# Optimization experiments

Hardware: AMD Instinct MI355X
Metric: run time of the kernel (lower is better)

## Reference

```python
import jax, jax.numpy as jnp
import numpy as np

N, DIM, K = 50000, 64, 16
POS_HID = 64
ATTN_HID = DIM * 4


def setup_inputs() -> dict:
    key = jax.random.key(0)
    ks = jax.random.split(key, 12)
    s = lambda fan_in: 1.0 / np.sqrt(fan_in)
    return {
        "x": jax.random.normal(ks[0], (N, DIM), jnp.float32),
        "pos": jax.random.normal(ks[1], (N, 3), jnp.float32),
        "attn_index": jax.random.randint(ks[2], (N, K), 0, N),
        "mask": jnp.zeros((N, K), dtype=bool),
        "w_qkv": jax.random.normal(ks[3], (DIM, 3 * DIM), jnp.float32) * s(DIM),
        "pm_w1": jax.random.normal(ks[4], (3, POS_HID), jnp.float32) * s(3),
        "pm_b1": jnp.zeros((POS_HID,), jnp.float32),
        "pm_w2": jax.random.normal(ks[5], (POS_HID, DIM), jnp.float32) * s(POS_HID),
        "pm_b2": jnp.zeros((DIM,), jnp.float32),
        "am_w1": jax.random.normal(ks[6], (DIM, ATTN_HID), jnp.float32) * s(DIM),
        "am_b1": jnp.zeros((ATTN_HID,), jnp.float32),
        "am_w2": jax.random.normal(ks[7], (ATTN_HID, DIM), jnp.float32) * s(ATTN_HID),
        "am_b2": jnp.zeros((DIM,), jnp.float32),
    }


def reference(x, pos, attn_index, mask, w_qkv, pm_w1, pm_b1, pm_w2, pm_b2,
              am_w1, am_b1, am_w2, am_b2):
    # qkv projection and split: [N, dim] each
    qkv = x @ w_qkv
    x_q, x_k, x_v = jnp.split(qkv, 3, axis=-1)

    # gather neighbors: [N, K, dim] / [N, K, 3]
    x_k = x_k[attn_index]
    x_v = x_v[attn_index]
    rel_pos = pos[attn_index] - pos[:, None, :]

    # positional MLP: 3 -> POS_HID -> dim
    rel = jax.nn.relu(rel_pos @ pm_w1 + pm_b1) @ pm_w2 + pm_b2

    # attention MLP on (k - q + rel): dim -> 4*dim -> dim
    w = x_k - x_q[:, None, :] + rel
    w = jax.nn.relu(w @ am_w1 + am_b1) @ am_w2 + am_b2

    # masked softmax over the neighbor dim (axis=1), per channel
    w = jnp.where(mask[:, :, None], -jnp.inf, w)
    w = jax.nn.softmax(w, axis=1)

    # weighted aggregation: [N, dim]
    agg = jnp.sum((x_v + rel) * w, axis=1)
    return agg
```

## Files before the change

### kernel.cpp

```cpp
#include <hip/hip_runtime.h>
#include <hip/hip_bf16.h>
#include <math.h>
#include <stdint.h>

#define DIM   64
#define KNB   16
#define QKVW  192
#define RVP   72
#define TFP   24

typedef short bf16x8 __attribute__((ext_vector_type(8)));
typedef float f32x4  __attribute__((ext_vector_type(4)));

__device__ __forceinline__ short f2bf_s(float x) {
    return (short)__builtin_bit_cast(unsigned short, __float2bfloat16(x));
}
__device__ __forceinline__ float bf2f(uint16_t u) {
    uint32_t v = ((uint32_t)u) << 16;
    return __builtin_bit_cast(float, v);
}

__global__ __launch_bounds__(256) void prep_kernel(
    const float* __restrict__ x, const float* __restrict__ wqkv,
    const float* __restrict__ am_w1, const float* __restrict__ am_w2,
    const float* __restrict__ pm_w2,
    uint16_t* __restrict__ qkvp, uint16_t* __restrict__ w1p,
    uint16_t* __restrict__ w2p, uint16_t* __restrict__ pw2p,
    int n, int nqkvb)
{
    const int tid = threadIdx.x;
    if (blockIdx.x < nqkvb) {
        const int w4   = tid >> 6;
        const int lane = tid & 63;
        const int g    = lane >> 4;
        const int nb   = lane & 15;
        const int r0   = blockIdx.x * 16;
        const int rowA = min(r0 + nb, n - 1);

        bf16x8 af[2];
#pragma unroll
        for (int kt = 0; kt < 2; ++kt) {
            const float* xr = x + (size_t)rowA * 64 + 32 * kt + 8 * g;
            const float4 a0 = *(const float4*)xr;
            const float4 a1 = *(const float4*)(xr + 4);
            bf16x8 f;
            f[0] = f2bf_s(a0.x); f[1] = f2bf_s(a0.y); f[2] = f2bf_s(a0.z); f[3] = f2bf_s(a0.w);
            f[4] = f2bf_s(a1.x); f[5] = f2bf_s(a1.y); f[6] = f2bf_s(a1.z); f[7] = f2bf_s(a1.w);
            af[kt] = f;
        }

#pragma unroll
        for (int t = 0; t < 3; ++t) {
            const int nt  = 3 * w4 + t;
            const int col = 16 * nt + nb;
            bf16x8 b0, b1;
#pragma unroll
            for (int j = 0; j < 8; ++j) {
                b0[j] = f2bf_s(wqkv[(8 * g + j) * QKVW + col]);
                b1[j] = f2bf_s(wqkv[(32 + 8 * g + j) * QKVW + col]);
            }
            f32x4 acc = {0.f, 0.f, 0.f, 0.f};
            acc = __builtin_amdgcn_mfma_f32_16x16x32_bf16(af[0], b0, acc, 0, 0, 0);
            acc = __builtin_amdgcn_mfma_f32_16x16x32_bf16(af[1], b1, acc, 0, 0, 0);
#pragma unroll
            for (int r = 0; r < 4; ++r) {
                const int row = r0 + 4 * g + r;
                if (row < n)
                    qkvp[(size_t)row * QKVW + col] = (uint16_t)f2bf_s(acc[r]);
            }
        }
    } else {
        int t = (blockIdx.x - nqkvb) * 256 + tid;
        if (t >= 36864) return;
        int j = t & 7, lane = (t >> 3) & 63, tile = t >> 9;
        int g = lane >> 4, nb = lane & 15;
        if (tile < 32) {
            int mt = tile >> 1, kt = tile & 1;
            w1p[t] = (uint16_t)f2bf_s(am_w1[(32 * kt + 8 * g + j) * 256 + 16 * mt + nb]);
        } else if (tile < 64) {
            int tt = tile - 32;
            int mt = tt >> 3, kt = tt & 7;
            w2p[t - 16384] = (uint16_t)f2bf_s(am_w2[(32 * kt + 8 * g + j) * 64 + 16 * mt + nb]);
        } else {
            int tt = tile - 64;
            int nt = tt >> 1, kt = tt & 1;
            pw2p[t - 32768] = (uint16_t)f2bf_s(pm_w2[(32 * kt + 8 * g + j) * 64 + 16 * nt + nb]);
        }
    }
}

__global__ __launch_bounds__(256, 2) void ptl_main(
    const float* __restrict__ pos,
    const int* __restrict__ aidx,
    const uint8_t* __restrict__ mask,
    const float* __restrict__ pm_w1,
    const float* __restrict__ pm_b1,
    const float* __restrict__ pm_b2,
    const float* __restrict__ am_b1,
    const uint16_t* __restrict__ qkvp,
    const uint16_t* __restrict__ w1p,
    const uint16_t* __restrict__ w2p,
    const uint16_t* __restrict__ pw2p,
    float* __restrict__ out,
    int npts)
{
    const int tid  = threadIdx.x;
    const int w    = tid >> 6;
    const int lane = tid & 63;
    const int g    = lane >> 4;
    const int nb   = lane & 15;

    __shared__ alignas(16) uint16_t s_rel[4][16][RVP];
    __shared__ alignas(16) uint16_t s_vrel[64][RVP];
    __shared__ alignas(16) uint16_t s_h2[64][256];
    __shared__ alignas(16) uint16_t s_tf[4][64][TFP];

    bf16x8 aw1[4][2], aw2[8];
#pragma unroll
    for (int m = 0; m < 4; ++m)
#pragma unroll
        for (int kt = 0; kt < 2; ++kt)
            aw1[m][kt] = *(const bf16x8*)(w1p + (size_t)(((4 * w + m) * 2 + kt) * 64 + lane) * 8);
#pragma unroll
    for (int kt = 0; kt < 8; ++kt)
        aw2[kt] = *(const bf16x8*)(w2p + (size_t)((w * 8 + kt) * 64 + lane) * 8);

    const int ngroups = (npts + 3) >> 2;

    int   pnw;
    float cx, cy, cz, prx, pry, prz;
    bf16x8 pk0, pk1;
    uint16_t pqv[4];

    auto stage_load = [&](int gbn) {
        const int gcl = min(gbn, ngroups - 1);
        const int ipn = min(gcl * 4 + w, npts - 1);
        pnw = aidx[ipn * KNB + nb];
        cx = pos[3 * ipn]; cy = pos[3 * ipn + 1]; cz = pos[3 * ipn + 2];
        prx = pos[3 * pnw]; pry = pos[3 * pnw + 1]; prz = pos[3 * pnw + 2];
        pk0 = *(const bf16x8*)(qkvp + (size_t)pnw * QKVW + 64 + 8 * g);
        pk1 = *(const bf16x8*)(qkvp + (size_t)pnw * QKVW + 96 + 8 * g);
#pragma unroll
        for (int nt = 0; nt < 4; ++nt)
            pqv[nt] = qkvp[(size_t)ipn * QKVW + 16 * nt + nb];
    };

    stage_load(blockIdx.x);

    for (int gb = blockIdx.x; gb < ngroups; gb += gridDim.x) {
        const int i0  = gb * 4;
        const int ipw = min(i0 + w, npts - 1);

        {
            const float rx = prx - cx, ry = pry - cy, rz = prz - cz;

            bf16x8 h1f[2];
#pragma unroll
            for (int kt = 0; kt < 2; ++kt) {
                const int hb = 32 * kt + 8 * g;
                float w0[8], w1r[8], w2r[8], bb[8];
                *(float4*)&w0[0]  = *(const float4*)(pm_w1 + hb);
                *(float4*)&w0[4]  = *(const float4*)(pm_w1 + hb + 4);
                *(float4*)&w1r[0] = *(const float4*)(pm_w1 + 64 + hb);
                *(float4*)&w1r[4] = *(const float4*)(pm_w1 + 64 + hb + 4);
                *(float4*)&w2r[0] = *(const float4*)(pm_w1 + 128 + hb);
                *(float4*)&w2r[4] = *(const float4*)(pm_w1 + 128 + hb + 4);
                *(float4*)&bb[0]  = *(const float4*)(pm_b1 + hb);
                *(float4*)&bb[4]  = *(const float4*)(pm_b1 + hb + 4);
                bf16x8 f;
#pragma unroll
                for (int jj = 0; jj < 8; ++jj) {
                    float v = fmaf(rx, w0[jj], fmaf(ry, w1r[jj], fmaf(rz, w2r[jj], bb[jj])));
                    f[jj] = f2bf_s(fmaxf(v, 0.f));
                }
                h1f[kt] = f;
            }
#pragma unroll
            for (int nt = 0; nt < 4; ++nt) {
                const bf16x8 b0 = *(const bf16x8*)(pw2p + (size_t)((nt * 2 + 0) * 64 + lane) * 8);
                const bf16x8 b1 = *(const bf16x8*)(pw2p + (size_t)((nt * 2 + 1) * 64 + lane) * 8);
                f32x4 acc = {0.f, 0.f, 0.f, 0.f};
                acc = __builtin_amdgcn_mfma_f32_16x16x32_bf16(h1f[0], b0, acc, 0, 0, 0);
                acc = __builtin_amdgcn_mfma_f32_16x16x32_bf16(h1f[1], b1, acc, 0, 0, 0);
                const int ch = 16 * nt + nb;
                const float bias = pm_b2[ch];
                const float qv = bf2f(pqv[nt]);
#pragma unroll
                for (int r = 0; r < 4; ++r)
                    s_rel[w][4 * g + r][ch] = (uint16_t)f2bf_s(acc[r] + bias - qv);
            }

            const bf16x8 rl0 = *(const bf16x8*)&s_rel[w][nb][8 * g];
            const bf16x8 rl1 = *(const bf16x8*)&s_rel[w][nb][32 + 8 * g];
            bf16x8 tf0, tf1;
#pragma unroll
            for (int j = 0; j < 8; ++j) {
                tf0[j] = f2bf_s(bf2f((uint16_t)pk0[j]) + bf2f((uint16_t)rl0[j]));
                tf1[j] = f2bf_s(bf2f((uint16_t)pk1[j]) + bf2f((uint16_t)rl1[j]));
            }
            *(bf16x8*)&s_tf[w][lane][0] = tf0;
            *(bf16x8*)&s_tf[w][lane][8] = tf1;
        }
        __syncthreads();

        {
            const bf16x8 pv0 = *(const bf16x8*)(qkvp + (size_t)pnw * QKVW + 128 + 8 * g);
            const bf16x8 pv1 = *(const bf16x8*)(qkvp + (size_t)pnw * QKVW + 160 + 8 * g);
            const bf16x8 pq0 = *(const bf16x8*)(qkvp + (size_t)ipw * QKVW + 8 * g);
            const bf16x8 pq1 = *(const bf16x8*)(qkvp + (size_t)ipw * QKVW + 32 + 8 * g);

#pragma unroll
            for (int pt = 0; pt < 4; ++pt) {
                const bf16x8 tf0 = *(const bf16x8*)&s_tf[pt][lane][0];
                const bf16x8 tf1 = *(const bf16x8*)&s_tf[pt][lane][8];

                f32x4 hacc[4];
                __builtin_amdgcn_s_setprio(1);
#pragma unroll
                for (int m = 0; m < 4; ++m) {
                    f32x4 a = {0.f, 0.f, 0.f, 0.f};
                    a = __builtin_amdgcn_mfma_f32_16x16x32_bf16(aw1[m][0], tf0, a, 0, 0, 0);
                    a = __builtin_amdgcn_mfma_f32_16x16x32_bf16(aw1[m][1], tf1, a, 0, 0, 0);
                    hacc[m] = a;
                }
                __builtin_amdgcn_s_setprio(0);
#pragma unroll
                for (int m = 0; m < 4; ++m) {
                    const int hb = 16 * (4 * w + m) + 4 * g;
                    const float4 b4 = *(const float4*)(am_b1 + hb);
                    const uint32_t lo = (uint32_t)(uint16_t)f2bf_s(fmaxf(hacc[m][0] + b4.x, 0.f))
                                      | ((uint32_t)(uint16_t)f2bf_s(fmaxf(hacc[m][1] + b4.y, 0.f)) << 16);
                    const uint32_t hi = (uint32_t)(uint16_t)f2bf_s(fmaxf(hacc[m][2] + b4.z, 0.f))
                                      | ((uint32_t)(uint16_t)f2bf_s(fmaxf(hacc[m][3] + b4.w, 0.f)) << 16);
                    const int sl = (2 * (4 * w + m) + (g >> 1)) ^ (nb & 7);
                    *(uint2*)((char*)&s_h2[16 * pt + nb][0] + sl * 16 + 8 * (g & 1)) = make_uint2(lo, hi);
                }
            }

            {
                const bf16x8 rl0 = *(const bf16x8*)&s_rel[w][nb][8 * g];
                const bf16x8 rl1 = *(const bf16x8*)&s_rel[w][nb][32 + 8 * g];
                bf16x8 va, vb;
#pragma unroll
                for (int j = 0; j < 8; ++j) {
                    va[j] = f2bf_s(bf2f((uint16_t)pv0[j]) + bf2f((uint16_t)rl0[j]) + bf2f((uint16_t)pq0[j]));
                    vb[j] = f2bf_s(bf2f((uint16_t)pv1[j]) + bf2f((uint16_t)rl1[j]) + bf2f((uint16_t)pq1[j]));
                }
                *(bf16x8*)&s_vrel[16 * w + nb][8 * g]      = va;
                *(bf16x8*)&s_vrel[16 * w + nb][32 + 8 * g] = vb;
            }
        }
        __syncthreads();

        stage_load(gb + gridDim.x);

#pragma unroll
        for (int mt = 0; mt < 4; ++mt) {
            const int ip  = i0 + mt;
            const int ipc = min(ip, npts - 1);

            f32x4 wacc = {0.f, 0.f, 0.f, 0.f};
            __builtin_amdgcn_s_setprio(1);
#pragma unroll
            for (int kt = 0; kt < 8; ++kt) {
                const int sl = (4 * kt + g) ^ (nb & 7);
                const bf16x8 a = *(const bf16x8*)((const char*)&s_h2[16 * mt + nb][0] + sl * 16);
                wacc = __builtin_amdgcn_mfma_f32_16x16x32_bf16(a, aw2[kt], wacc, 0, 0, 0);
            }
            __builtin_amdgcn_s_setprio(0);

            const uchar4 m4 = *(const uchar4*)(mask + (size_t)ipc * KNB + 4 * g);
            const float sc0 = m4.x ? -INFINITY : wacc[0];
            const float sc1 = m4.y ? -INFINITY : wacc[1];
            const float sc2 = m4.z ? -INFINITY : wacc[2];
            const float sc3 = m4.w ? -INFINITY : wacc[3];
            float mx = fmaxf(fmaxf(sc0, sc1), fmaxf(sc2, sc3));
            mx = fmaxf(mx, __shfl_xor(mx, 16));
            mx = fmaxf(mx, __shfl_xor(mx, 32));
            const float e0 = __expf(sc0 - mx), e1 = __expf(sc1 - mx);
            const float e2 = __expf(sc2 - mx), e3 = __expf(sc3 - mx);
            float den = (e0 + e1) + (e2 + e3);

            const int vc = 16 * w + nb;
            const float vr0 = bf2f(s_vrel[16 * mt + 4 * g + 0][vc]);
            const float vr1 = bf2f(s_vrel[16 * mt + 4 * g + 1][vc]);
            const float vr2 = bf2f(s_vrel[16 * mt + 4 * g + 2][vc]);
            const float vr3 = bf2f(s_vrel[16 * mt + 4 * g + 3][vc]);
            float num = e0 * vr0;
            num = fmaf(e1, vr1, num);
            num = fmaf(e2, vr2, num);
            num = fmaf(e3, vr3, num);

            den += __shfl_xor(den, 16); den += __shfl_xor(den, 32);
            num += __shfl_xor(num, 16); num += __shfl_xor(num, 32);
            if (lane < 16 && ip < npts)
                out[(size_t)ip * 64 + vc] = __fdividef(num, den);
        }
    }
}

extern "C" void kernel_launch(void* const* d_in, const int* in_sizes, int n_in,
                              void* d_out, int out_size, void* d_ws, size_t ws_size,
                              hipStream_t stream) {
    const float*   x     = (const float*)d_in[0];
    const float*   pos   = (const float*)d_in[1];
    const int*     aidx  = (const int*)d_in[2];
    const uint8_t* mask  = (const uint8_t*)d_in[3];
    const float*   wqkv  = (const float*)d_in[4];
    const float*   pm_w1 = (const float*)d_in[5];
    const float*   pm_b1 = (const float*)d_in[6];
    const float*   pm_w2 = (const float*)d_in[7];
    const float*   pm_b2 = (const float*)d_in[8];
    const float*   am_w1 = (const float*)d_in[9];
    const float*   am_b1 = (const float*)d_in[10];
    const float*   am_w2 = (const float*)d_in[11];
    float* out = (float*)d_out;
    const int n = in_sizes[0] / DIM;

    uint8_t* ws = (uint8_t*)d_ws;
    uint16_t* qkvp = (uint16_t*)ws;
    uint16_t* w1p  = (uint16_t*)(ws + (size_t)n * QKVW * 2);
    uint16_t* w2p  = w1p + 16384;
    uint16_t* pw2p = w2p + 16384;

    const int nqkvb = (n + 15) / 16;
    prep_kernel<<<nqkvb + 144, 256, 0, stream>>>(x, wqkv, am_w1, am_w2, pm_w2,
                                                 qkvp, w1p, w2p, pw2p, n, nqkvb);
    ptl_main<<<512, 256, 0, stream>>>(pos, aidx, mask, pm_w1, pm_b1, pm_b2, am_b1,
                                      qkvp, w1p, w2p, pw2p, out, n);
}
```

Before: 160.0 us.

## Halve hidden-activation LDS buffer and process points in two phases for occupancy

The per-block hidden-activation shared buffer is halved and the s_tf row padding is reduced, cutting LDS per block so more blocks fit per CU. The grid grows from 512 to 768 blocks to use the extra occupancy. To make the smaller buffer work, the first-MLP/MFMA stage and the second-MLP/softmax stage now each run on two points at a time, alternating, with the v+rel staging split by wave halves. The cost is two extra block barriers per iteration, and the tighter s_tf padding may add LDS bank conflicts.

```diff
diff --git a/kernel.cpp b/kernel.cpp
--- a/kernel.cpp
+++ b/kernel.cpp
@@ -7,7 +7,7 @@
 #define KNB   16
 #define QKVW  192
 #define RVP   72
-#define TFP   24
+#define TFP   16
 
 typedef short bf16x8 __attribute__((ext_vector_type(8)));
 typedef float f32x4  __attribute__((ext_vector_type(4)));
@@ -112,7 +112,7 @@
 
     __shared__ alignas(16) uint16_t s_rel[4][16][RVP];
     __shared__ alignas(16) uint16_t s_vrel[64][RVP];
-    __shared__ alignas(16) uint16_t s_h2[64][256];
+    __shared__ alignas(16) uint16_t s_h2h[32][256];
     __shared__ alignas(16) uint16_t s_tf[4][64][TFP];
 
     bf16x8 aw1[4][2], aw2[8];
@@ -150,6 +150,103 @@
     for (int gb = blockIdx.x; gb < ngroups; gb += gridDim.x) {
         const int i0  = gb * 4;
         const int ipw = min(i0 + w, npts - 1);
+
+        auto P2half = [&](int pt0) {
+            const bool own = (w & 2) == pt0;
+            bf16x8 pv0_, pv1_, pq0_, pq1_;
+            if (own) {
+                pv0_ = *(const bf16x8*)(qkvp + (size_t)pnw * QKVW + 128 + 8 * g);
+                pv1_ = *(const bf16x8*)(qkvp + (size_t)pnw * QKVW + 160 + 8 * g);
+                pq0_ = *(const bf16x8*)(qkvp + (size_t)ipw * QKVW + 8 * g);
+                pq1_ = *(const bf16x8*)(qkvp + (size_t)ipw * QKVW + 32 + 8 * g);
+            }
+#pragma unroll
+            for (int ptl = 0; ptl < 2; ++ptl) {
+                const int pt = pt0 + ptl;
+                const bf16x8 tf0 = *(const bf16x8*)&s_tf[pt][lane][0];
+                const bf16x8 tf1 = *(const bf16x8*)&s_tf[pt][lane][8];
+
+                f32x4 hacc[4];
+                __builtin_amdgcn_s_setprio(1);
+#pragma unroll
+                for (int m = 0; m < 4; ++m) {
+                    f32x4 a = {0.f, 0.f, 0.f, 0.f};
+                    a = __builtin_amdgcn_mfma_f32_16x16x32_bf16(aw1[m][0], tf0, a, 0, 0, 0);
+                    a = __builtin_amdgcn_mfma_f32_16x16x32_bf16(aw1[m][1], tf1, a, 0, 0, 0);
+                    hacc[m] = a;
+                }
+                __builtin_amdgcn_s_setprio(0);
+#pragma unroll
+                for (int m = 0; m < 4; ++m) {
+                    const int hb = 16 * (4 * w + m) + 4 * g;
+                    const float4 b4 = *(const float4*)(am_b1 + hb);
+                    const uint32_t lo = (uint32_t)(uint16_t)f2bf_s(fmaxf(hacc[m][0] + b4.x, 0.f))
+                                      | ((uint32_t)(uint16_t)f2bf_s(fmaxf(hacc[m][1] + b4.y, 0.f)) << 16);
+                    const uint32_t hi = (uint32_t)(uint16_t)f2bf_s(fmaxf(hacc[m][2] + b4.z, 0.f))
+                                      | ((uint32_t)(uint16_t)f2bf_s(fmaxf(hacc[m][3] + b4.w, 0.f)) << 16);
+                    const int sl = (2 * (4 * w + m) + (g >> 1)) ^ (nb & 7);
+                    *(uint2*)((char*)&s_h2h[16 * ptl + nb][0] + sl * 16 + 8 * (g & 1)) = make_uint2(lo, hi);
+                }
+            }
+            if (own) {
+                const bf16x8 rl0 = *(const bf16x8*)&s_rel[w][nb][8 * g];
+                const bf16x8 rl1 = *(const bf16x8*)&s_rel[w][nb][32 + 8 * g];
+                bf16x8 va, vb;
+#pragma unroll
+                for (int j = 0; j < 8; ++j) {
+                    va[j] = f2bf_s(bf2f((uint16_t)pv0_[j]) + bf2f((uint16_t)rl0[j]) + bf2f((uint16_t)pq0_[j]));
+                    vb[j] = f2bf_s(bf2f((uint16_t)pv1_[j]) + bf2f((uint16_t)rl1[j]) + bf2f((uint16_t)pq1_[j]));
+                }
+                *(bf16x8*)&s_vrel[16 * w + nb][8 * g]      = va;
+                *(bf16x8*)&s_vrel[16 * w + nb][32 + 8 * g] = vb;
+            }
+        };
+
+        auto P3half = [&](int pt0) {
+#pragma unroll
+            for (int mi = 0; mi < 2; ++mi) {
+                const int mt  = pt0 + mi;
+                const int ip  = i0 + mt;
+                const int ipc = min(ip, npts - 1);
+
+                f32x4 wacc = {0.f, 0.f, 0.f, 0.f};
+                __builtin_amdgcn_s_setprio(1);
+#pragma unroll
+                for (int kt = 0; kt < 8; ++kt) {
+                    const int sl = (4 * kt + g) ^ (nb & 7);
+                    const bf16x8 a = *(const bf16x8*)((const char*)&s_h2h[16 * mi + nb][0] + sl * 16);
+                    wacc = __builtin_amdgcn_mfma_f32_16x16x32_bf16(a, aw2[kt], wacc, 0, 0, 0);
+                }
+                __builtin_amdgcn_s_setprio(0);
+
+                const uchar4 m4 = *(const uchar4*)(mask + (size_t)ipc * KNB + 4 * g);
+                const float sc0 = m4.x ? -INFINITY : wacc[0];
+                const float sc1 = m4.y ? -INFINITY : wacc[1];
+                const float sc2 = m4.z ? -INFINITY : wacc[2];
+                const float sc3 = m4.w ? -INFINITY : wacc[3];
+                float mx = fmaxf(fmaxf(sc0, sc1), fmaxf(sc2, sc3));
+                mx = fmaxf(mx, __shfl_xor(mx, 16));
+                mx = fmaxf(mx, __shfl_xor(mx, 32));
+                const float e0 = __expf(sc0 - mx), e1 = __expf(sc1 - mx);
+                const float e2 = __expf(sc2 - mx), e3 = __expf(sc3 - mx);
+                float den = (e0 + e1) + (e2 + e3);
+
+                const int vc = 16 * w + nb;
+                const float vr0 = bf2f(s_vrel[16 * mt + 4 * g + 0][vc]);
+                const float vr1 = bf2f(s_vrel[16 * mt + 4 * g + 1][vc]);
+                const float vr2 = bf2f(s_vrel[16 * mt + 4 * g + 2][vc]);
+                const float vr3 = bf2f(s_vrel[16 * mt + 4 * g + 3][vc]);
+                float num = e0 * vr0;
+                num = fmaf(e1, vr1, num);
+                num = fmaf(e2, vr2, num);
+                num = fmaf(e3, vr3, num);
+
+                den += __shfl_xor(den, 16); den += __shfl_xor(den, 32);
+                num += __shfl_xor(num, 16); num += __shfl_xor(num, 32);
+                if (lane < 16 && ip < npts)
+                    out[(size_t)ip * 64 + vc] = __fdividef(num, den);
+            }
+        };
 
         {
             const float rx = prx - cx, ry = pry - cy, rz = prz - cz;
@@ -203,99 +300,14 @@
         }
         __syncthreads();
 
-        {
-            const bf16x8 pv0 = *(const bf16x8*)(qkvp + (size_t)pnw * QKVW + 128 + 8 * g);
-            const bf16x8 pv1 = *(const bf16x8*)(qkvp + (size_t)pnw * QKVW + 160 + 8 * g);
-            const bf16x8 pq0 = *(const bf16x8*)(qkvp + (size_t)ipw * QKVW + 8 * g);
-            const bf16x8 pq1 = *(const bf16x8*)(qkvp + (size_t)ipw * QKVW + 32 + 8 * g);
-
-#pragma unroll
-            for (int pt = 0; pt < 4; ++pt) {
-                const bf16x8 tf0 = *(const bf16x8*)&s_tf[pt][lane][0];
-                const bf16x8 tf1 = *(const bf16x8*)&s_tf[pt][lane][8];
-
-                f32x4 hacc[4];
-                __builtin_amdgcn_s_setprio(1);
-#pragma unroll
-                for (int m = 0; m < 4; ++m) {
-                    f32x4 a = {0.f, 0.f, 0.f, 0.f};
-                    a = __builtin_amdgcn_mfma_f32_16x16x32_bf16(aw1[m][0], tf0, a, 0, 0, 0);
-                    a = __builtin_amdgcn_mfma_f32_16x16x32_bf16(aw1[m][1], tf1, a, 0, 0, 0);
-                    hacc[m] = a;
-                }
-                __builtin_amdgcn_s_setprio(0);
-#pragma unroll
-                for (int m = 0; m < 4; ++m) {
-                    const int hb = 16 * (4 * w + m) + 4 * g;
-                    const float4 b4 = *(const float4*)(am_b1 + hb);
-                    const uint32_t lo = (uint32_t)(uint16_t)f2bf_s(fmaxf(hacc[m][0] + b4.x, 0.f))
-                                      | ((uint32_t)(uint16_t)f2bf_s(fmaxf(hacc[m][1] + b4.y, 0.f)) << 16);
-                    const uint32_t hi = (uint32_t)(uint16_t)f2bf_s(fmaxf(hacc[m][2] + b4.z, 0.f))
-                                      | ((uint32_t)(uint16_t)f2bf_s(fmaxf(hacc[m][3] + b4.w, 0.f)) << 16);
-                    const int sl = (2 * (4 * w + m) + (g >> 1)) ^ (nb & 7);
-                    *(uint2*)((char*)&s_h2[16 * pt + nb][0] + sl * 16 + 8 * (g & 1)) = make_uint2(lo, hi);
-                }
-            }
-
-            {
-                const bf16x8 rl0 = *(const bf16x8*)&s_rel[w][nb][8 * g];
-                const bf16x8 rl1 = *(const bf16x8*)&s_rel[w][nb][32 + 8 * g];
-                bf16x8 va, vb;
-#pragma unroll
-                for (int j = 0; j < 8; ++j) {
-                    va[j] = f2bf_s(bf2f((uint16_t)pv0[j]) + bf2f((uint16_t)rl0[j]) + bf2f((uint16_t)pq0[j]));
-                    vb[j] = f2bf_s(bf2f((uint16_t)pv1[j]) + bf2f((uint16_t)rl1[j]) + bf2f((uint16_t)pq1[j]));
-                }
-                *(bf16x8*)&s_vrel[16 * w + nb][8 * g]      = va;
-                *(bf16x8*)&s_vrel[16 * w + nb][32 + 8 * g] = vb;
-            }
-        }
+        P2half(0);
         __syncthreads();
-
+        P3half(0);
+        __syncthreads();
+        P2half(2);
+        __syncthreads();
         stage_load(gb + gridDim.x);
-
-#pragma unroll
-        for (int mt = 0; mt < 4; ++mt) {
-            const int ip  = i0 + mt;
-            const int ipc = min(ip, npts - 1);
-
-            f32x4 wacc = {0.f, 0.f, 0.f, 0.f};
-            __builtin_amdgcn_s_setprio(1);
-#pragma unroll
-            for (int kt = 0; kt < 8; ++kt) {
-                const int sl = (4 * kt + g) ^ (nb & 7);
-                const bf16x8 a = *(const bf16x8*)((const char*)&s_h2[16 * mt + nb][0] + sl * 16);
-                wacc = __builtin_amdgcn_mfma_f32_16x16x32_bf16(a, aw2[kt], wacc, 0, 0, 0);
-            }
-            __builtin_amdgcn_s_setprio(0);
-
-            const uchar4 m4 = *(const uchar4*)(mask + (size_t)ipc * KNB + 4 * g);
-            const float sc0 = m4.x ? -INFINITY : wacc[0];
-            const float sc1 = m4.y ? -INFINITY : wacc[1];
-            const float sc2 = m4.z ? -INFINITY : wacc[2];
-            const float sc3 = m4.w ? -INFINITY : wacc[3];
-            float mx = fmaxf(fmaxf(sc0, sc1), fmaxf(sc2, sc3));
-            mx = fmaxf(mx, __shfl_xor(mx, 16));
-            mx = fmaxf(mx, __shfl_xor(mx, 32));
-            const float e0 = __expf(sc0 - mx), e1 = __expf(sc1 - mx);
-            const float e2 = __expf(sc2 - mx), e3 = __expf(sc3 - mx);
-            float den = (e0 + e1) + (e2 + e3);
-
-            const int vc = 16 * w + nb;
-            const float vr0 = bf2f(s_vrel[16 * mt + 4 * g + 0][vc]);
-            const float vr1 = bf2f(s_vrel[16 * mt + 4 * g + 1][vc]);
-            const float vr2 = bf2f(s_vrel[16 * mt + 4 * g + 2][vc]);
-            const float vr3 = bf2f(s_vrel[16 * mt + 4 * g + 3][vc]);
-            float num = e0 * vr0;
-            num = fmaf(e1, vr1, num);
-            num = fmaf(e2, vr2, num);
-            num = fmaf(e3, vr3, num);
-
-            den += __shfl_xor(den, 16); den += __shfl_xor(den, 32);
-            num += __shfl_xor(num, 16); num += __shfl_xor(num, 32);
-            if (lane < 16 && ip < npts)
-                out[(size_t)ip * 64 + vc] = __fdividef(num, den);
-        }
+        P3half(2);
     }
 }
 
@@ -326,6 +338,6 @@
     const int nqkvb = (n + 15) / 16;
     prep_kernel<<<nqkvb + 144, 256, 0, stream>>>(x, wqkv, am_w1, am_w2, pm_w2,
                                                  qkvp, w1p, w2p, pw2p, n, nqkvb);
-    ptl_main<<<512, 256, 0, stream>>>(pos, aidx, mask, pm_w1, pm_b1, pm_b2, am_b1,
+    ptl_main<<<768, 256, 0, stream>>>(pos, aidx, mask, pm_w1, pm_b1, pm_b2, am_b1,
                                       qkvp, w1p, w2p, pw2p, out, n);
 }
```

New measurement: 201.9 us. 1.26x slower.
